# Kernel optimization log

Hardware: AMD Instinct MI355X
Metric: run time of the kernel (lower is better)

The kernel has to match this reference:

```python
import jax, jax.numpy as jnp
import numpy as np

NEG_SLOPE = 0.2

def gat_layer(x, src, dst, W, a_src, a_dst, b):
    # PyG GATConv (concat=True, self-loops already appended to src/dst)
    N = x.shape[0]
    H, C = a_src.shape
    h = (x @ W).reshape(N, H, C)                      # [N,H,C]
    alpha_s = jnp.einsum('nhc,hc->nh', h, a_src)      # [N,H]
    alpha_d = jnp.einsum('nhc,hc->nh', h, a_dst)
    e = jax.nn.leaky_relu(alpha_s[src] + alpha_d[dst], NEG_SLOPE)  # [E,H]
    # scatter-softmax over edges grouped by destination node
    m = jax.ops.segment_max(e, dst, num_segments=N)
    e = jnp.exp(e - m[dst])
    denom = jax.ops.segment_sum(e, dst, num_segments=N)
    alpha = e / (denom[dst] + 1e-16)                  # [E,H]
    msg = h[src] * alpha[:, :, None]                  # [E,H,C]
    out = jax.ops.segment_sum(msg, dst, num_segments=N)
    return out.reshape(N, H * C) + b


def setup_inputs() -> dict:
    key = jax.random.key(0)
    ks = jax.random.split(key, 16)
    N, E, B = 20000, 640000, 32
    in_f, out_dim = 128, 512
    x = jax.random.normal(ks[0], (N, in_f), dtype=jnp.float32)
    edge_index = jax.random.randint(ks[1], (2, E), 0, N, dtype=jnp.int64)
    batch = jnp.sort(jax.random.randint(ks[2], (N,), 0, B, dtype=jnp.int64))
    def p(k, shape):
        return jax.random.normal(k, shape, dtype=jnp.float32) * 0.1
    inp = {
        'x': x, 'edge_index': edge_index, 'batch': batch,
        'W1': p(ks[3], (in_f, 256)), 'a1_src': p(ks[4], (4, 64)), 'a1_dst': p(ks[5], (4, 64)), 'b1': jnp.zeros((256,), jnp.float32),
        'W2': p(ks[6], (256, 256)), 'a2_src': p(ks[7], (4, 64)), 'a2_dst': p(ks[8], (4, 64)), 'b2': jnp.zeros((256,), jnp.float32),
        'W3': p(ks[9], (256, 256)), 'a3_src': p(ks[10], (4, 64)), 'a3_dst': p(ks[11], (4, 64)), 'b3': jnp.zeros((256,), jnp.float32),
        'W4': p(ks[12], (256, 512)), 'a4_src': p(ks[13], (4, 128)), 'a4_dst': p(ks[14], (4, 128)), 'b4': jnp.zeros((512,), jnp.float32),
        'fcW': p(ks[15], (1024, out_dim)), 'fcb': jnp.zeros((out_dim,), jnp.float32),
    }
    return inp


def reference(x, edge_index, batch, W1, a1_src, a1_dst, b1, W2, a2_src, a2_dst, b2,
              W3, a3_src, a3_dst, b3, W4, a4_src, a4_dst, b4, fcW, fcb):
    N = x.shape[0]
    B = 32
    loops = jnp.arange(N, dtype=edge_index.dtype)
    src = jnp.concatenate([edge_index[0], loops])
    dst = jnp.concatenate([edge_index[1], loops])
    h = jax.nn.elu(gat_layer(x, src, dst, W1, a1_src, a1_dst, b1))
    h = jax.nn.elu(gat_layer(h, src, dst, W2, a2_src, a2_dst, b2))
    h = jax.nn.elu(gat_layer(h, src, dst, W3, a3_src, a3_dst, b3))
    h = jax.nn.elu(gat_layer(h, src, dst, W4, a4_src, a4_dst, b4))   # [N,512]
    cnt = jax.ops.segment_sum(jnp.ones((N,), h.dtype), batch, num_segments=B)
    x_mean = jax.ops.segment_sum(h, batch, num_segments=B) / jnp.maximum(cnt, 1.0)[:, None]
    x_max = jax.ops.segment_max(h, batch, num_segments=B)
    x_max = jnp.where(jnp.isfinite(x_max), x_max, 0.0)
    g = jnp.concatenate([x_mean, x_max], axis=1)                     # [B,1024]
    return g @ fcW + fcb
```

## Files before the change

kernel.cpp:

```cpp
#include <hip/hip_runtime.h>
#include <math.h>

#define WAVE 64

typedef __attribute__((ext_vector_type(8))) short short8v;
typedef __attribute__((ext_vector_type(4))) float f32x4;
typedef _Float16 h16x4 __attribute__((ext_vector_type(4)));
typedef _Float16 h16x8 __attribute__((ext_vector_type(8)));

__device__ __forceinline__ unsigned short f2b(float x){
  unsigned u = __float_as_uint(x);
  unsigned r = u + 0x7fffu + ((u >> 16) & 1u);
  return (unsigned short)(r >> 16);
}
__device__ __forceinline__ float b2f(unsigned short h){
  return __uint_as_float(((unsigned)h) << 16);
}
__device__ __forceinline__ float selh(float e0, float e1, float e2, float e3, int m){
  float r = (m == 1) ? e1 : e0;
  r = (m == 2) ? e2 : r;
  r = (m == 3) ? e3 : r;
  return r;
}

__global__ void k_zero_i(int* p, int n){
  int i = blockIdx.x*blockDim.x + threadIdx.x;
  if (i < n) p[i] = 0;
}

__global__ void k_zero_f(float* p, int n){
  int i = blockIdx.x*blockDim.x + threadIdx.x;
  if (i < n) p[i] = 0.f;
}

__global__ void k_count(const int* __restrict__ ei, int E, int N, int* __restrict__ cnt){
  int i = blockIdx.x*blockDim.x + threadIdx.x;
  if (i >= E + N) return;
  int d = (i < E) ? ei[E + i] : (i - E);
  atomicAdd(&cnt[d], 1);
}

__global__ __launch_bounds__(1024)
void k_scan1(const int* __restrict__ cnt, int* __restrict__ rp, int* __restrict__ bsum, int N){
  __shared__ int sd[1024];
  int t = threadIdx.x, i = blockIdx.x*1024 + t;
  int v = (i < N) ? cnt[i] : 0;
  sd[t] = v;
  __syncthreads();
  for (int off = 1; off < 1024; off <<= 1){
    int x = (t >= off) ? sd[t-off] : 0;
    __syncthreads();
    sd[t] += x;
    __syncthreads();
  }
  if (i < N) rp[i] = sd[t] - v;
  if (t == 1023) bsum[blockIdx.x] = sd[1023];
}

__global__ void k_scan2(int* __restrict__ bsum, int nb, int* __restrict__ rp, int N){
  int t = threadIdx.x;
  int orig = (t < nb) ? bsum[t] : 0;
  int v = orig;
  #pragma unroll
  for (int off = 1; off < 64; off <<= 1){
    int x = __shfl_up(v, off, WAVE);
    if (t >= off) v += x;
  }
  if (t < nb) bsum[t] = v - orig;
  if (t == 63) rp[N] = v;
}

__global__ __launch_bounds__(1024)
void k_scan3(int* __restrict__ rp, const int* __restrict__ bsum, int N){
  int i = blockIdx.x*1024 + threadIdx.x;
  if (i < N) rp[i] += bsum[blockIdx.x];
}

__global__ void k_copy_i(const int* __restrict__ a, int* __restrict__ b, int n){
  int i = blockIdx.x*blockDim.x + threadIdx.x;
  if (i < n) b[i] = a[i];
}

__global__ void k_fill(const int* __restrict__ ei, int E, int N,
                       int* __restrict__ cur, int* __restrict__ es){
  int i = blockIdx.x*blockDim.x + threadIdx.x;
  if (i >= E + N) return;
  int s, d;
  if (i < E){ s = ei[i]; d = ei[E + i]; } else { s = d = i - E; }
  int pos = atomicAdd(&cur[d], 1);
  es[pos] = s;
}

__global__ void k_bounds(const int* __restrict__ batch, int N, int B, int* __restrict__ bs){
  int b = blockIdx.x*blockDim.x + threadIdx.x;
  if (b > B) return;
  int lo = 0, hi = N;
  while (lo < hi){ int mid = (lo + hi) >> 1; if (batch[mid] < b) lo = mid + 1; else hi = mid; }
  bs[b] = lo;
}

__global__ __launch_bounds__(256)
void k_cvt(const float* __restrict__ in, unsigned short* __restrict__ hi,
           unsigned short* __restrict__ lo, int n4){
  int i = blockIdx.x*blockDim.x + threadIdx.x;
  if (i >= n4) return;
  float4 v = ((const float4*)in)[i];
  ushort4 h, l;
  h.x = f2b(v.x); l.x = f2b(v.x - b2f(h.x));
  h.y = f2b(v.y); l.y = f2b(v.y - b2f(h.y));
  h.z = f2b(v.z); l.z = f2b(v.z - b2f(h.z));
  h.w = f2b(v.w); l.w = f2b(v.w - b2f(h.w));
  ((ushort4*)hi)[i] = h;
  ((ushort4*)lo)[i] = l;
}

__global__ __launch_bounds__(256)
void k_cvt_w(const float* __restrict__ W, unsigned short* __restrict__ th,
             unsigned short* __restrict__ tl, int K, int Nc){
  int i = blockIdx.x*blockDim.x + threadIdx.x;
  if (i >= K*Nc) return;
  int k = i / Nc, n = i - k*Nc;
  float a = W[i];
  unsigned short h = f2b(a);
  unsigned short l = f2b(a - b2f(h));
  th[(size_t)n*K + k] = h;
  tl[(size_t)n*K + k] = l;
}

template<int CHEAD>
__global__ __launch_bounds__(256)
void k_gemm_fused(const unsigned short* __restrict__ Ah, const unsigned short* __restrict__ Al,
                  const unsigned short* __restrict__ Bh, const unsigned short* __restrict__ Bl,
                  _Float16* __restrict__ Ch,
                  const float* __restrict__ asr, const float* __restrict__ adt,
                  float* __restrict__ as4, float* __restrict__ ad4,
                  int M, int K, int Nc){
  constexpr int LDP = 40;
  __shared__ unsigned short sAh[64*LDP], sAl[64*LDP], sBh[64*LDP], sBl[64*LDP];
  const int tid = threadIdx.x;
  const int m0 = blockIdx.x*64, n0 = blockIdx.y*64;
  const int w = tid >> 6, l = tid & 63;
  const int sr = tid >> 2, sc = (tid & 3)*8;
  f32x4 acc0 = {0.f,0.f,0.f,0.f}, acc1 = acc0, acc2 = acc0, acc3 = acc0;
  const int arow = m0 + sr;
  const bool aval = arow < M;
  const size_t aoff = (size_t)arow*K + sc;
  const size_t boff = (size_t)(n0 + sr)*K + sc;
  const int fa = (w*16 + (l & 15))*LDP + (l >> 4)*8;
  const int fb = (l & 15)*LDP + (l >> 4)*8;

  for (int k0 = 0; k0 < K; k0 += 32){
    uint4 z = make_uint4(0,0,0,0);
    uint4 va_h = z, va_l = z;
    if (aval){
      va_h = *(const uint4*)(Ah + aoff + k0);
      va_l = *(const uint4*)(Al + aoff + k0);
    }
    uint4 vb_h = *(const uint4*)(Bh + boff + k0);
    uint4 vb_l = *(const uint4*)(Bl + boff + k0);
    __syncthreads();
    *(uint4*)&sAh[sr*LDP + sc] = va_h;
    *(uint4*)&sAl[sr*LDP + sc] = va_l;
    *(uint4*)&sBh[sr*LDP + sc] = vb_h;
    *(uint4*)&sBl[sr*LDP + sc] = vb_l;
    __syncthreads();

    short8v a_h = *(const short8v*)&sAh[fa];
    short8v a_l = *(const short8v*)&sAl[fa];

    short8v b_h, b_l;
    b_h = *(const short8v*)&sBh[fb];
    b_l = *(const short8v*)&sBl[fb];
    acc0 = __builtin_amdgcn_mfma_f32_16x16x32_bf16(a_h, b_h, acc0, 0, 0, 0);
    acc0 = __builtin_amdgcn_mfma_f32_16x16x32_bf16(a_h, b_l, acc0, 0, 0, 0);
    acc0 = __builtin_amdgcn_mfma_f32_16x16x32_bf16(a_l, b_h, acc0, 0, 0, 0);

    b_h = *(const short8v*)&sBh[fb + 16*LDP];
    b_l = *(const short8v*)&sBl[fb + 16*LDP];
    acc1 = __builtin_amdgcn_mfma_f32_16x16x32_bf16(a_h, b_h, acc1, 0, 0, 0);
    acc1 = __builtin_amdgcn_mfma_f32_16x16x32_bf16(a_h, b_l, acc1, 0, 0, 0);
    acc1 = __builtin_amdgcn_mfma_f32_16x16x32_bf16(a_l, b_h, acc1, 0, 0, 0);

    b_h = *(const short8v*)&sBh[fb + 32*LDP];
    b_l = *(const short8v*)&sBl[fb + 32*LDP];
    acc2 = __builtin_amdgcn_mfma_f32_16x16x32_bf16(a_h, b_h, acc2, 0, 0, 0);
    acc2 = __builtin_amdgcn_mfma_f32_16x16x32_bf16(a_h, b_l, acc2, 0, 0, 0);
    acc2 = __builtin_amdgcn_mfma_f32_16x16x32_bf16(a_l, b_h, acc2, 0, 0, 0);

    b_h = *(const short8v*)&sBh[fb + 48*LDP];
    b_l = *(const short8v*)&sBl[fb + 48*LDP];
    acc3 = __builtin_amdgcn_mfma_f32_16x16x32_bf16(a_h, b_h, acc3, 0, 0, 0);
    acc3 = __builtin_amdgcn_mfma_f32_16x16x32_bf16(a_h, b_l, acc3, 0, 0, 0);
    acc3 = __builtin_amdgcn_mfma_f32_16x16x32_bf16(a_l, b_h, acc3, 0, 0, 0);
    __syncthreads();
  }

  const int rb = m0 + w*16 + (l >> 4)*4;
  const int cb = n0 + (l & 15);

  #pragma unroll
  for (int j = 0; j < 4; ++j){
    int row = rb + j;
    if (row < M){
      _Float16* hp = Ch + (size_t)row*Nc + cb;
      hp[0]  = (_Float16)acc0[j];
      hp[16] = (_Float16)acc1[j];
      hp[32] = (_Float16)acc2[j];
      hp[48] = (_Float16)acc3[j];
    }
  }

  const int hy = n0 / CHEAD;
  const float ca0 = asr[cb], ca1 = asr[cb+16], ca2 = asr[cb+32], ca3 = asr[cb+48];
  const float cd0 = adt[cb], cd1 = adt[cb+16], cd2 = adt[cb+32], cd3 = adt[cb+48];
  #pragma unroll
  for (int j = 0; j < 4; ++j){
    float ps = ca0*acc0[j] + ca1*acc1[j] + ca2*acc2[j] + ca3*acc3[j];
    float pd = cd0*acc0[j] + cd1*acc1[j] + cd2*acc2[j] + cd3*acc3[j];
    ps += __shfl_xor(ps, 1, WAVE);  pd += __shfl_xor(pd, 1, WAVE);
    ps += __shfl_xor(ps, 2, WAVE);  pd += __shfl_xor(pd, 2, WAVE);
    ps += __shfl_xor(ps, 4, WAVE);  pd += __shfl_xor(pd, 4, WAVE);
    ps += __shfl_xor(ps, 8, WAVE);  pd += __shfl_xor(pd, 8, WAVE);
    int row = rb + j;
    if ((l & 15) == 0 && row < M){
      atomicAdd(&as4[(size_t)row*4 + hy], ps);
      atomicAdd(&ad4[(size_t)row*4 + hy], pd);
    }
  }
}

template<int HC, int WF32>
__global__ __launch_bounds__(256)
void k_agg_h(const int* __restrict__ rp, const int* __restrict__ es,
             const float* __restrict__ as4, const float* __restrict__ ad4,
             const _Float16* __restrict__ h, const float* __restrict__ bias,
             float* __restrict__ outF,
             unsigned short* __restrict__ oAh, unsigned short* __restrict__ oAl, int N){
  constexpr int VEC = HC / 64;
  int wid  = (blockIdx.x*blockDim.x + threadIdx.x) >> 6;
  int lane = threadIdx.x & 63;
  if (wid >= N) return;
  int beg = rp[wid], end = rp[wid+1];

  const float4 adv = *(const float4*)(ad4 + (size_t)wid*4);
  const float ad0 = adv.x, ad1 = adv.y, ad2 = adv.z, ad3 = adv.w;

  float m0=-1e30f, m1=-1e30f, m2=-1e30f, m3=-1e30f;
  float s0=0.f, s1=0.f, s2=0.f, s3=0.f;
  for (int i = beg + lane; i < end; i += WAVE){
    int s = es[i];
    const float4 av = *(const float4*)(as4 + (size_t)s*4);
    float e, mn;
    e = av.x + ad0; e = (e >= 0.f) ? e : 0.2f*e;
    mn = fmaxf(m0, e); s0 = s0*__expf(m0-mn) + __expf(e-mn); m0 = mn;
    e = av.y + ad1; e = (e >= 0.f) ? e : 0.2f*e;
    mn = fmaxf(m1, e); s1 = s1*__expf(m1-mn) + __expf(e-mn); m1 = mn;
    e = av.z + ad2; e = (e >= 0.f) ? e : 0.2f*e;
    mn = fmaxf(m2, e); s2 = s2*__expf(m2-mn) + __expf(e-mn); m2 = mn;
    e = av.w + ad3; e = (e >= 0.f) ? e : 0.2f*e;
    mn = fmaxf(m3, e); s3 = s3*__expf(m3-mn) + __expf(e-mn); m3 = mn;
  }
  #pragma unroll
  for (int off = 32; off > 0; off >>= 1){
    float mo, so, mn;
    mo = __shfl_xor(m0, off, WAVE); so = __shfl_xor(s0, off, WAVE);
    mn = fmaxf(m0, mo); s0 = s0*__expf(m0-mn) + so*__expf(mo-mn); m0 = mn;
    mo = __shfl_xor(m1, off, WAVE); so = __shfl_xor(s1, off, WAVE);
    mn = fmaxf(m1, mo); s1 = s1*__expf(m1-mn) + so*__expf(mo-mn); m1 = mn;
    mo = __shfl_xor(m2, off, WAVE); so = __shfl_xor(s2, off, WAVE);
    mn = fmaxf(m2, mo); s2 = s2*__expf(m2-mn) + so*__expf(mo-mn); m2 = mn;
    mo = __shfl_xor(m3, off, WAVE); so = __shfl_xor(s3, off, WAVE);
    mn = fmaxf(m3, mo); s3 = s3*__expf(m3-mn) + so*__expf(mo-mn); m3 = mn;
  }
  const float i0 = 1.f/(s0 + 1e-16f), i1 = 1.f/(s1 + 1e-16f);
  const float i2 = 1.f/(s2 + 1e-16f), i3 = 1.f/(s3 + 1e-16f);
  const int myh = lane >> 4;

  float ac[VEC] = {};

  for (int cb = beg; cb < end; cb += WAVE){
    int nn = min(WAVE, end - cb);
    int sidx = 0;
    float w0 = 0.f, w1 = 0.f, w2 = 0.f, w3 = 0.f;
    if (cb + lane < end){
      sidx = es[cb + lane];
      const float4 av = *(const float4*)(as4 + (size_t)sidx*4);
      float e;
      e = av.x + ad0; e = (e >= 0.f) ? e : 0.2f*e; w0 = __expf(e - m0)*i0;
      e = av.y + ad1; e = (e >= 0.f) ? e : 0.2f*e; w1 = __expf(e - m1)*i1;
      e = av.z + ad2; e = (e >= 0.f) ? e : 0.2f*e; w2 = __expf(e - m2)*i2;
      e = av.w + ad3; e = (e >= 0.f) ? e : 0.2f*e; w3 = __expf(e - m3)*i3;
    }

    int j = 0;
    for (; j + 4 <= nn; j += 4){
      int sj0 = __shfl(sidx, j+0, WAVE), sj1 = __shfl(sidx, j+1, WAVE);
      int sj2 = __shfl(sidx, j+2, WAVE), sj3 = __shfl(sidx, j+3, WAVE);
      float u0 = selh(__shfl(w0,j+0,WAVE), __shfl(w1,j+0,WAVE), __shfl(w2,j+0,WAVE), __shfl(w3,j+0,WAVE), myh);
      float u1 = selh(__shfl(w0,j+1,WAVE), __shfl(w1,j+1,WAVE), __shfl(w2,j+1,WAVE), __shfl(w3,j+1,WAVE), myh);
      float u2 = selh(__shfl(w0,j+2,WAVE), __shfl(w1,j+2,WAVE), __shfl(w2,j+2,WAVE), __shfl(w3,j+2,WAVE), myh);
      float u3 = selh(__shfl(w0,j+3,WAVE), __shfl(w1,j+3,WAVE), __shfl(w2,j+3,WAVE), __shfl(w3,j+3,WAVE), myh);
      if (VEC == 4){
        h16x4 v0 = *(const h16x4*)(h + (size_t)sj0*HC + lane*4);
        h16x4 v1 = *(const h16x4*)(h + (size_t)sj1*HC + lane*4);
        h16x4 v2 = *(const h16x4*)(h + (size_t)sj2*HC + lane*4);
        h16x4 v3 = *(const h16x4*)(h + (size_t)sj3*HC + lane*4);
        #pragma unroll
        for (int c = 0; c < 4; ++c)
          ac[c] = fmaf(u0,(float)v0[c], fmaf(u1,(float)v1[c], fmaf(u2,(float)v2[c], fmaf(u3,(float)v3[c], ac[c]))));
      } else {
        h16x8 v0 = *(const h16x8*)(h + (size_t)sj0*HC + lane*8);
        h16x8 v1 = *(const h16x8*)(h + (size_t)sj1*HC + lane*8);
        h16x8 v2 = *(const h16x8*)(h + (size_t)sj2*HC + lane*8);
        h16x8 v3 = *(const h16x8*)(h + (size_t)sj3*HC + lane*8);
        #pragma unroll
        for (int c = 0; c < VEC; ++c)
          ac[c] = fmaf(u0,(float)v0[c], fmaf(u1,(float)v1[c], fmaf(u2,(float)v2[c], fmaf(u3,(float)v3[c], ac[c]))));
      }
    }
    for (; j < nn; ++j){
      int sj = __shfl(sidx, j, WAVE);
      float u = selh(__shfl(w0,j,WAVE), __shfl(w1,j,WAVE), __shfl(w2,j,WAVE), __shfl(w3,j,WAVE), myh);
      if (VEC == 4){
        h16x4 v = *(const h16x4*)(h + (size_t)sj*HC + lane*4);
        #pragma unroll
        for (int c = 0; c < 4; ++c) ac[c] = fmaf(u, (float)v[c], ac[c]);
      } else {
        h16x8 v = *(const h16x8*)(h + (size_t)sj*HC + lane*8);
        #pragma unroll
        for (int c = 0; c < VEC; ++c) ac[c] = fmaf(u, (float)v[c], ac[c]);
      }
    }
  }

  float r0=0,r1=0,r2=0,r3=0,r4=0,r5=0,r6=0,r7=0;
  {
    const float* bp = bias + lane*VEC;
    #pragma unroll
    for (int c = 0; c < VEC; ++c){
      float r = ac[c] + bp[c];
      r = r > 0.f ? r : expm1f(r);
      if (c==0) r0=r; else if (c==1) r1=r; else if (c==2) r2=r; else if (c==3) r3=r;
      else if (c==4) r4=r; else if (c==5) r5=r; else if (c==6) r6=r; else r7=r;
    }
  }
  if (WF32){
    float* op = outF + (size_t)wid*HC + lane*VEC;
    *(float4*)op = make_float4(r0,r1,r2,r3);
    if (VEC == 8) *(float4*)(op+4) = make_float4(r4,r5,r6,r7);
  } else {
    ushort4 H, L;
    H.x = f2b(r0); L.x = f2b(r0 - b2f(H.x));
    H.y = f2b(r1); L.y = f2b(r1 - b2f(H.y));
    H.z = f2b(r2); L.z = f2b(r2 - b2f(H.z));
    H.w = f2b(r3); L.w = f2b(r3 - b2f(H.w));
    *(ushort4*)(oAh + (size_t)wid*HC + lane*VEC) = H;
    *(ushort4*)(oAl + (size_t)wid*HC + lane*VEC) = L;
    if (VEC == 8){
      ushort4 H2, L2;
      H2.x = f2b(r4); L2.x = f2b(r4 - b2f(H2.x));
      H2.y = f2b(r5); L2.y = f2b(r5 - b2f(H2.y));
      H2.z = f2b(r6); L2.z = f2b(r6 - b2f(H2.z));
      H2.w = f2b(r7); L2.w = f2b(r7 - b2f(H2.w));
      *(ushort4*)(oAh + (size_t)wid*HC + lane*VEC + 4) = H2;
      *(ushort4*)(oAl + (size_t)wid*HC + lane*VEC + 4) = L2;
    }
  }
}

__global__ void k_pool_partial(const float* __restrict__ h, const int* __restrict__ bs,
                               float* __restrict__ psum, float* __restrict__ pmax){
  int b = blockIdx.x, ch = blockIdx.y;
  int f = threadIdx.x;
  int s = bs[b], e = bs[b+1];
  long long len = e - s;
  int i0 = s + (int)(len * ch / 8);
  int i1 = s + (int)(len * (ch+1) / 8);
  float sm = 0.f, mx = -3.0e38f;
  for (int i = i0; i < i1; ++i){
    float v = h[(size_t)i*512 + f];
    sm += v; mx = fmaxf(mx, v);
  }
  int idx = (b*8 + ch)*512 + f;
  psum[idx] = sm; pmax[idx] = mx;
}

__global__ void k_pool_final(const float* __restrict__ psum, const float* __restrict__ pmax,
                             const int* __restrict__ bs, float* __restrict__ g){
  int b = blockIdx.x, f = threadIdx.x;
  float sm = 0.f, mx = -3.0e38f;
  for (int c = 0; c < 8; ++c){
    int idx = (b*8 + c)*512 + f;
    sm += psum[idx]; mx = fmaxf(mx, pmax[idx]);
  }
  int cnt = bs[b+1] - bs[b];
  g[b*1024 + f] = sm / fmaxf((float)cnt, 1.f);
  g[b*1024 + 512 + f] = (mx > -1e37f) ? mx : 0.f;
}

__global__ __launch_bounds__(256)
void k_fc(const float* __restrict__ g, const float* __restrict__ fcW,
          const float* __restrict__ fcb, float* __restrict__ out){
  __shared__ float gs[1024];
  __shared__ float red[4][64];
  int b = blockIdx.x, t = threadIdx.x;
  int o0 = blockIdx.y * 64;
  for (int i = t; i < 1024; i += 256) gs[i] = g[b*1024 + i];
  __syncthreads();
  int ol = t & 63, q = t >> 6;
  const float* wp = fcW + (size_t)(q*256)*512 + o0 + ol;
  float acc = 0.f;
  #pragma unroll 8
  for (int k = 0; k < 256; ++k)
    acc = fmaf(gs[q*256 + k], wp[(size_t)k*512], acc);
  red[q][ol] = acc;
  __syncthreads();
  if (t < 64){
    float r = red[0][t] + red[1][t] + red[2][t] + red[3][t] + fcb[o0 + t];
    out[b*512 + o0 + t] = r;
  }
}

extern "C" void kernel_launch(void* const* d_in, const int* in_sizes, int n_in,
                              void* d_out, int out_size, void* d_ws, size_t ws_size,
                              hipStream_t stream){
  (void)n_in; (void)out_size; (void)ws_size;
  const float* x     = (const float*)d_in[0];
  const int*   ei    = (const int*)d_in[1];
  const int*   batch = (const int*)d_in[2];
  const float* W[4]   = {(const float*)d_in[3],(const float*)d_in[7],(const float*)d_in[11],(const float*)d_in[15]};
  const float* asr[4] = {(const float*)d_in[4],(const float*)d_in[8],(const float*)d_in[12],(const float*)d_in[16]};
  const float* adt[4] = {(const float*)d_in[5],(const float*)d_in[9],(const float*)d_in[13],(const float*)d_in[17]};
  const float* bb[4]  = {(const float*)d_in[6],(const float*)d_in[10],(const float*)d_in[14],(const float*)d_in[18]};
  const float* fcW = (const float*)d_in[19];
  const float* fcb = (const float*)d_in[20];

  const int N  = in_sizes[0] / 128;
  const int E  = in_sizes[1] / 2;
  const int EN = E + N;
  const int B  = 32;
  const int NB = (N + 1023) / 1024;

  char* p = (char*)d_ws;
  auto alloc = [&](size_t bytes){ void* r = (void*)p; p += (bytes + 255) & ~(size_t)255; return r; };
  float* bufA = (float*)alloc((size_t)N*512*4);
  _Float16* bufH = (_Float16*)alloc((size_t)N*512*2);
  unsigned short* Ah = (unsigned short*)alloc((size_t)N*256*2);
  unsigned short* Al = (unsigned short*)alloc((size_t)N*256*2);
  unsigned short* Wh = (unsigned short*)alloc((size_t)512*256*2);
  unsigned short* Wl = (unsigned short*)alloc((size_t)512*256*2);
  float* a2   = (float*)alloc((size_t)N*8*4);
  float* as4 = a2;
  float* ad4 = a2 + (size_t)N*4;
  int*   cnt  = (int*)alloc((size_t)N*4);
  int*   rp   = (int*)alloc((size_t)(N+1)*4);
  int*   cur  = (int*)alloc((size_t)N*4);
  int*   es   = (int*)alloc((size_t)EN*4);
  int*   bs   = (int*)alloc((size_t)(B+1)*4);
  int*   bsum = (int*)alloc((size_t)64*4);
  float* gpo  = (float*)alloc((size_t)B*1024*4);
  float* psum = (float*)alloc((size_t)B*8*512*4);
  float* pmax = (float*)alloc((size_t)B*8*512*4);

  k_zero_i<<<(N+255)/256, 256, 0, stream>>>(cnt, N);
  k_count<<<(EN+255)/256, 256, 0, stream>>>(ei, E, N, cnt);
  k_scan1<<<NB, 1024, 0, stream>>>(cnt, rp, bsum, N);
  k_scan2<<<1, 64, 0, stream>>>(bsum, NB, rp, N);
  k_scan3<<<NB, 1024, 0, stream>>>(rp, bsum, N);
  k_copy_i<<<(N+255)/256, 256, 0, stream>>>(rp, cur, N);
  k_fill<<<(EN+255)/256, 256, 0, stream>>>(ei, E, N, cur, es);
  k_bounds<<<1, 64, 0, stream>>>(batch, N, B, bs);

  const int wgrid = (N + 3) / 4;

  k_cvt<<<((N*128/4) + 255)/256, 256, 0, stream>>>(x, Ah, Al, N*128/4);

  const int Kd[4]  = {128, 256, 256, 256};
  const int HCd[4] = {256, 256, 256, 512};

  for (int L = 0; L < 4; ++L){
    const int K = Kd[L], Nc = HCd[L];
    k_zero_f<<<(N*8 + 255)/256, 256, 0, stream>>>(a2, N*8);
    k_cvt_w<<<(K*Nc + 255)/256, 256, 0, stream>>>(W[L], Wh, Wl, K, Nc);
    dim3 gg((N + 63)/64, Nc/64);
    if (Nc == 256)
      k_gemm_fused<64><<<gg, 256, 0, stream>>>(Ah, Al, Wh, Wl, bufH, asr[L], adt[L], as4, ad4, N, K, Nc);
    else
      k_gemm_fused<128><<<gg, 256, 0, stream>>>(Ah, Al, Wh, Wl, bufH, asr[L], adt[L], as4, ad4, N, K, Nc);
    if (L < 3)
      k_agg_h<256,0><<<wgrid, 256, 0, stream>>>(rp, es, as4, ad4, bufH, bb[L], (float*)nullptr, Ah, Al, N);
    else
      k_agg_h<512,1><<<wgrid, 256, 0, stream>>>(rp, es, as4, ad4, bufH, bb[L], bufA, (unsigned short*)nullptr, (unsigned short*)nullptr, N);
  }

  dim3 pg(B, 8);
  k_pool_partial<<<pg, 512, 0, stream>>>(bufA, bs, psum, pmax);
  k_pool_final<<<B, 512, 0, stream>>>(psum, pmax, bs, gpo);
  dim3 fg(B, 8);
  k_fc<<<fg, 256, 0, stream>>>(gpo, fcW, fcb, (float*)d_out);
}
```

Baseline: 512.3 us.

## Enlarge fused GEMM tile to 128x128 with 8 waves and 2x4 fragments

The split-bf16 fused GEMM now uses 128x128 output tiles with 512 threads. Each wave computes a 32x64 sub-tile, reusing each loaded B fragment across two A fragments. This halves the number of blocks and raises arithmetic per shared-memory load. The redundant end-of-loop barrier is dropped, since the barrier before the shared-memory stores already protects reuse. The trade-off is fewer blocks on a large GPU and more registers per thread, which may reduce occupancy.

```diff
diff --git a/kernel.cpp b/kernel.cpp
--- a/kernel.cpp
+++ b/kernel.cpp
@@ -128,7 +128,7 @@
 }
 
 template<int CHEAD>
-__global__ __launch_bounds__(256)
+__global__ __launch_bounds__(512)
 void k_gemm_fused(const unsigned short* __restrict__ Ah, const unsigned short* __restrict__ Al,
                   const unsigned short* __restrict__ Bh, const unsigned short* __restrict__ Bl,
                   _Float16* __restrict__ Ch,
@@ -136,18 +136,24 @@
                   float* __restrict__ as4, float* __restrict__ ad4,
                   int M, int K, int Nc){
   constexpr int LDP = 40;
-  __shared__ unsigned short sAh[64*LDP], sAl[64*LDP], sBh[64*LDP], sBl[64*LDP];
+  __shared__ unsigned short sAh[128*LDP], sAl[128*LDP], sBh[128*LDP], sBl[128*LDP];
   const int tid = threadIdx.x;
-  const int m0 = blockIdx.x*64, n0 = blockIdx.y*64;
+  const int m0 = blockIdx.x*128, n0 = blockIdx.y*128;
   const int w = tid >> 6, l = tid & 63;
+  const int wr = w >> 1, wc = w & 1;
   const int sr = tid >> 2, sc = (tid & 3)*8;
-  f32x4 acc0 = {0.f,0.f,0.f,0.f}, acc1 = acc0, acc2 = acc0, acc3 = acc0;
+
+  f32x4 acc00={0.f,0.f,0.f,0.f}, acc01=acc00, acc02=acc00, acc03=acc00;
+  f32x4 acc10=acc00, acc11=acc00, acc12=acc00, acc13=acc00;
+
   const int arow = m0 + sr;
   const bool aval = arow < M;
   const size_t aoff = (size_t)arow*K + sc;
   const size_t boff = (size_t)(n0 + sr)*K + sc;
-  const int fa = (w*16 + (l & 15))*LDP + (l >> 4)*8;
-  const int fb = (l & 15)*LDP + (l >> 4)*8;
+
+  const int fa0 = (wr*32 + (l & 15))*LDP + (l >> 4)*8;
+  const int fa1 = fa0 + 16*LDP;
+  const int fb0 = (wc*64 + (l & 15))*LDP + (l >> 4)*8;
 
   for (int k0 = 0; k0 < K; k0 += 32){
     uint4 z = make_uint4(0,0,0,0);
@@ -165,66 +171,100 @@
     *(uint4*)&sBl[sr*LDP + sc] = vb_l;
     __syncthreads();
 
-    short8v a_h = *(const short8v*)&sAh[fa];
-    short8v a_l = *(const short8v*)&sAl[fa];
+    short8v a_h0 = *(const short8v*)&sAh[fa0];
+    short8v a_l0 = *(const short8v*)&sAl[fa0];
+    short8v a_h1 = *(const short8v*)&sAh[fa1];
+    short8v a_l1 = *(const short8v*)&sAl[fa1];
 
     short8v b_h, b_l;
-    b_h = *(const short8v*)&sBh[fb];
-    b_l = *(const short8v*)&sBl[fb];
-    acc0 = __builtin_amdgcn_mfma_f32_16x16x32_bf16(a_h, b_h, acc0, 0, 0, 0);
-    acc0 = __builtin_amdgcn_mfma_f32_16x16x32_bf16(a_h, b_l, acc0, 0, 0, 0);
-    acc0 = __builtin_amdgcn_mfma_f32_16x16x32_bf16(a_l, b_h, acc0, 0, 0, 0);
-
-    b_h = *(const short8v*)&sBh[fb + 16*LDP];
-    b_l = *(const short8v*)&sBl[fb + 16*LDP];
-    acc1 = __builtin_amdgcn_mfma_f32_16x16x32_bf16(a_h, b_h, acc1, 0, 0, 0);
-    acc1 = __builtin_amdgcn_mfma_f32_16x16x32_bf16(a_h, b_l, acc1, 0, 0, 0);
-    acc1 = __builtin_amdgcn_mfma_f32_16x16x32_bf16(a_l, b_h, acc1, 0, 0, 0);
-
-    b_h = *(const short8v*)&sBh[fb + 32*LDP];
-    b_l = *(const short8v*)&sBl[fb + 32*LDP];
-    acc2 = __builtin_amdgcn_mfma_f32_16x16x32_bf16(a_h, b_h, acc2, 0, 0, 0);
-    acc2 = __builtin_amdgcn_mfma_f32_16x16x32_bf16(a_h, b_l, acc2, 0, 0, 0);
-    acc2 = __builtin_amdgcn_mfma_f32_16x16x32_bf16(a_l, b_h, acc2, 0, 0, 0);
-
-    b_h = *(const short8v*)&sBh[fb + 48*LDP];
-    b_l = *(const short8v*)&sBl[fb + 48*LDP];
-    acc3 = __builtin_amdgcn_mfma_f32_16x16x32_bf16(a_h, b_h, acc3, 0, 0, 0);
-    acc3 = __builtin_amdgcn_mfma_f32_16x16x32_bf16(a_h, b_l, acc3, 0, 0, 0);
-    acc3 = __builtin_amdgcn_mfma_f32_16x16x32_bf16(a_l, b_h, acc3, 0, 0, 0);
-    __syncthreads();
-  }
-
-  const int rb = m0 + w*16 + (l >> 4)*4;
-  const int cb = n0 + (l & 15);
-
-  #pragma unroll
-  for (int j = 0; j < 4; ++j){
-    int row = rb + j;
-    if (row < M){
-      _Float16* hp = Ch + (size_t)row*Nc + cb;
-      hp[0]  = (_Float16)acc0[j];
-      hp[16] = (_Float16)acc1[j];
-      hp[32] = (_Float16)acc2[j];
-      hp[48] = (_Float16)acc3[j];
-    }
-  }
-
-  const int hy = n0 / CHEAD;
-  const float ca0 = asr[cb], ca1 = asr[cb+16], ca2 = asr[cb+32], ca3 = asr[cb+48];
-  const float cd0 = adt[cb], cd1 = adt[cb+16], cd2 = adt[cb+32], cd3 = adt[cb+48];
-  #pragma unroll
-  for (int j = 0; j < 4; ++j){
-    float ps = ca0*acc0[j] + ca1*acc1[j] + ca2*acc2[j] + ca3*acc3[j];
-    float pd = cd0*acc0[j] + cd1*acc1[j] + cd2*acc2[j] + cd3*acc3[j];
-    ps += __shfl_xor(ps, 1, WAVE);  pd += __shfl_xor(pd, 1, WAVE);
-    ps += __shfl_xor(ps, 2, WAVE);  pd += __shfl_xor(pd, 2, WAVE);
-    ps += __shfl_xor(ps, 4, WAVE);  pd += __shfl_xor(pd, 4, WAVE);
-    ps += __shfl_xor(ps, 8, WAVE);  pd += __shfl_xor(pd, 8, WAVE);
-    int row = rb + j;
-    if ((l & 15) == 0 && row < M){
-      atomicAdd(&as4[(size_t)row*4 + hy], ps);
-      atomicAdd(&ad4[(size_t)row*4 + hy], pd);
+    b_h = *(const short8v*)&sBh[fb0];
+    b_l = *(const short8v*)&sBl[fb0];
+    acc00 = __builtin_amdgcn_mfma_f32_16x16x32_bf16(a_h0, b_h, acc00, 0, 0, 0);
+    acc00 = __builtin_amdgcn_mfma_f32_16x16x32_bf16(a_h0, b_l, acc00, 0, 0, 0);
+    acc00 = __builtin_amdgcn_mfma_f32_16x16x32_bf16(a_l0, b_h, acc00, 0, 0, 0);
+    acc10 = __builtin_amdgcn_mfma_f32_16x16x32_bf16(a_h1, b_h, acc10, 0, 0, 0);
+    acc10 = __builtin_amdgcn_mfma_f32_16x16x32_bf16(a_h1, b_l, acc10, 0, 0, 0);
+    acc10 = __builtin_amdgcn_mfma_f32_16x16x32_bf16(a_l1, b_h, acc10, 0, 0, 0);
+
+    b_h = *(const short8v*)&sBh[fb0 + 16*LDP];
+    b_l = *(const short8v*)&sBl[fb0 + 16*LDP];
+    acc01 = __builtin_amdgcn_mfma_f32_16x16x32_bf16(a_h0, b_h, acc01, 0, 0, 0);
+    acc01 = __builtin_amdgcn_mfma_f32_16x16x32_bf16(a_h0, b_l, acc01, 0, 0, 0);
+    acc01 = __builtin_amdgcn_mfma_f32_16x16x32_bf16(a_l0, b_h, acc01, 0, 0, 0);
+    acc11 = __builtin_amdgcn_mfma_f32_16x16x32_bf16(a_h1, b_h, acc11, 0, 0, 0);
+    acc11 = __builtin_amdgcn_mfma_f32_16x16x32_bf16(a_h1, b_l, acc11, 0, 0, 0);
+    acc11 = __builtin_amdgcn_mfma_f32_16x16x32_bf16(a_l1, b_h, acc11, 0, 0, 0);
+
+    b_h = *(const short8v*)&sBh[fb0 + 32*LDP];
+    b_l = *(const short8v*)&sBl[fb0 + 32*LDP];
+    acc02 = __builtin_amdgcn_mfma_f32_16x16x32_bf16(a_h0, b_h, acc02, 0, 0, 0);
+    acc02 = __builtin_amdgcn_mfma_f32_16x16x32_bf16(a_h0, b_l, acc02, 0, 0, 0);
+    acc02 = __builtin_amdgcn_mfma_f32_16x16x32_bf16(a_l0, b_h, acc02, 0, 0, 0);
+    acc12 = __builtin_amdgcn_mfma_f32_16x16x32_bf16(a_h1, b_h, acc12, 0, 0, 0);
+    acc12 = __builtin_amdgcn_mfma_f32_16x16x32_bf16(a_h1, b_l, acc12, 0, 0, 0);
+    acc12 = __builtin_amdgcn_mfma_f32_16x16x32_bf16(a_l1, b_h, acc12, 0, 0, 0);
+
+    b_h = *(const short8v*)&sBh[fb0 + 48*LDP];
+    b_l = *(const short8v*)&sBl[fb0 + 48*LDP];
+    acc03 = __builtin_amdgcn_mfma_f32_16x16x32_bf16(a_h0, b_h, acc03, 0, 0, 0);
+    acc03 = __builtin_amdgcn_mfma_f32_16x16x32_bf16(a_h0, b_l, acc03, 0, 0, 0);
+    acc03 = __builtin_amdgcn_mfma_f32_16x16x32_bf16(a_l0, b_h, acc03, 0, 0, 0);
+    acc13 = __builtin_amdgcn_mfma_f32_16x16x32_bf16(a_h1, b_h, acc13, 0, 0, 0);
+    acc13 = __builtin_amdgcn_mfma_f32_16x16x32_bf16(a_h1, b_l, acc13, 0, 0, 0);
+    acc13 = __builtin_amdgcn_mfma_f32_16x16x32_bf16(a_l1, b_h, acc13, 0, 0, 0);
+  }
+
+  const int colb = n0 + wc*64 + (l & 15);
+  const int hy = (n0 + wc*64) / CHEAD;
+  const float ca0 = asr[colb], ca1 = asr[colb+16], ca2 = asr[colb+32], ca3 = asr[colb+48];
+  const float cd0 = adt[colb], cd1 = adt[colb+16], cd2 = adt[colb+32], cd3 = adt[colb+48];
+
+  {
+    const int rb = m0 + wr*32 + (l >> 4)*4;
+    #pragma unroll
+    for (int j = 0; j < 4; ++j){
+      int row = rb + j;
+      if (row < M){
+        _Float16* hp = Ch + (size_t)row*Nc + colb;
+        hp[0]  = (_Float16)acc00[j];
+        hp[16] = (_Float16)acc01[j];
+        hp[32] = (_Float16)acc02[j];
+        hp[48] = (_Float16)acc03[j];
+      }
+      float ps = ca0*acc00[j] + ca1*acc01[j] + ca2*acc02[j] + ca3*acc03[j];
+      float pd = cd0*acc00[j] + cd1*acc01[j] + cd2*acc02[j] + cd3*acc03[j];
+      ps += __shfl_xor(ps, 1, WAVE);  pd += __shfl_xor(pd, 1, WAVE);
+      ps += __shfl_xor(ps, 2, WAVE);  pd += __shfl_xor(pd, 2, WAVE);
+      ps += __shfl_xor(ps, 4, WAVE);  pd += __shfl_xor(pd, 4, WAVE);
+      ps += __shfl_xor(ps, 8, WAVE);  pd += __shfl_xor(pd, 8, WAVE);
+      if ((l & 15) == 0 && row < M){
+        atomicAdd(&as4[(size_t)row*4 + hy], ps);
+        atomicAdd(&ad4[(size_t)row*4 + hy], pd);
+      }
+    }
+  }
+  {
+    const int rb = m0 + wr*32 + 16 + (l >> 4)*4;
+    #pragma unroll
+    for (int j = 0; j < 4; ++j){
+      int row = rb + j;
+      if (row < M){
+        _Float16* hp = Ch + (size_t)row*Nc + colb;
+        hp[0]  = (_Float16)acc10[j];
+        hp[16] = (_Float16)acc11[j];
+        hp[32] = (_Float16)acc12[j];
+        hp[48] = (_Float16)acc13[j];
+      }
+      float ps = ca0*acc10[j] + ca1*acc11[j] + ca2*acc12[j] + ca3*acc13[j];
+      float pd = cd0*acc10[j] + cd1*acc11[j] + cd2*acc12[j] + cd3*acc13[j];
+      ps += __shfl_xor(ps, 1, WAVE);  pd += __shfl_xor(pd, 1, WAVE);
+      ps += __shfl_xor(ps, 2, WAVE);  pd += __shfl_xor(pd, 2, WAVE);
+      ps += __shfl_xor(ps, 4, WAVE);  pd += __shfl_xor(pd, 4, WAVE);
+      ps += __shfl_xor(ps, 8, WAVE);  pd += __shfl_xor(pd, 8, WAVE);
+      if ((l & 15) == 0 && row < M){
+        atomicAdd(&as4[(size_t)row*4 + hy], ps);
+        atomicAdd(&ad4[(size_t)row*4 + hy], pd);
+      }
     }
   }
 }
@@ -482,11 +522,11 @@
     const int K = Kd[L], Nc = HCd[L];
     k_zero_f<<<(N*8 + 255)/256, 256, 0, stream>>>(a2, N*8);
     k_cvt_w<<<(K*Nc + 255)/256, 256, 0, stream>>>(W[L], Wh, Wl, K, Nc);
-    dim3 gg((N + 63)/64, Nc/64);
+    dim3 gg((N + 127)/128, Nc/128);
     if (Nc == 256)
-      k_gemm_fused<64><<<gg, 256, 0, stream>>>(Ah, Al, Wh, Wl, bufH, asr[L], adt[L], as4, ad4, N, K, Nc);
+      k_gemm_fused<64><<<gg, 512, 0, stream>>>(Ah, Al, Wh, Wl, bufH, asr[L], adt[L], as4, ad4, N, K, Nc);
     else
-      k_gemm_fused<128><<<gg, 256, 0, stream>>>(Ah, Al, Wh, Wl, bufH, asr[L], adt[L], as4, ad4, N, K, Nc);
+      k_gemm_fused<128><<<gg, 512, 0, stream>>>(Ah, Al, Wh, Wl, bufH, asr[L], adt[L], as4, ad4, N, K, Nc);
     if (L < 3)
       k_agg_h<256,0><<<wgrid, 256, 0, stream>>>(rp, es, as4, ad4, bufH, bb[L], (float*)nullptr, Ah, Al, N);
     else
```

New measurement: 509.6 us. About the same (-0.5%).
